# Performance work log

Measured on AMD Instinct MI355X. Metric: run time of the kernel, lower is better.

The kernel has to match this reference:

```python
import jax, jax.numpy as jnp
import numpy as np

EMB = 768
HEADS = 12
HEAD_DIM = EMB // HEADS
SEQ = 4096
BATCH = 1


def setup_inputs() -> dict:
    key = jax.random.key(0)
    ks = jax.random.split(key, 9)
    s = 1.0 / np.sqrt(EMB)
    return {
        "x": jax.random.normal(ks[0], (BATCH, SEQ, EMB), dtype=jnp.float32),
        "wq": jax.random.normal(ks[1], (EMB, EMB), dtype=jnp.float32) * s,
        "bq": jax.random.normal(ks[2], (EMB,), dtype=jnp.float32) * s,
        "wk": jax.random.normal(ks[3], (EMB, EMB), dtype=jnp.float32) * s,
        "bk": jax.random.normal(ks[4], (EMB,), dtype=jnp.float32) * s,
        "wv": jax.random.normal(ks[5], (EMB, EMB), dtype=jnp.float32) * s,
        "bv": jax.random.normal(ks[6], (EMB,), dtype=jnp.float32) * s,
        "wo": jax.random.normal(ks[7], (EMB, EMB), dtype=jnp.float32) * s,
        "bo": jax.random.normal(ks[8], (EMB,), dtype=jnp.float32) * s,
    }


def reference(x, wq, bq, wk, bk, wv, bv, wo, bo):
    b, n, _ = x.shape
    # projections: [b, n, emb] -> [b, heads, n, head_dim]
    def split_heads(t):
        return t.reshape(b, n, HEADS, HEAD_DIM).transpose(0, 2, 1, 3)
    q = split_heads(x @ wq + bq)
    k = split_heads(x @ wk + bk)
    v = split_heads(x @ wv + bv)
    # full N x N scores (naive attention, as in the original)
    scores = jnp.einsum("bhqd,bhkd->bhqk", q, k)
    causal = jnp.triu(jnp.ones((n, n), dtype=bool), k=1)
    scores = jnp.where(causal, -jnp.inf, scores)
    weights = jax.nn.softmax(scores / np.sqrt(HEAD_DIM), axis=-1)
    # dropout with rate 0.0 is identity (eval mode)
    ctx = jnp.einsum("bhqk,bhkd->bhqd", weights, v)
    ctx = ctx.transpose(0, 2, 1, 3).reshape(b, n, EMB)
    return ctx @ wo + bo
```

## Files before the change

### kernel.cpp

```cpp
#include <hip/hip_runtime.h>
#include <stdint.h>

#define SEQ 4096
#define EMB 768
#define HEADS 12
#define HD 64

typedef __attribute__((ext_vector_type(8))) short short8;
typedef __attribute__((ext_vector_type(4))) short short4v;
typedef __attribute__((ext_vector_type(8))) __bf16 bf16x8;
typedef __attribute__((ext_vector_type(4))) __bf16 bf16x4;
typedef __attribute__((ext_vector_type(4))) float f32x4;

#define QSCALE 0.18033688011112043f

static __device__ __forceinline__ unsigned short f2bf(float f) {
    unsigned int u = __builtin_bit_cast(unsigned int, f);
    unsigned int r = 0x7fffu + ((u >> 16) & 1u);
    u += r;
    return (unsigned short)(u >> 16);
}

static __device__ __forceinline__ f32x4 mfma32(short8 a, short8 b, f32x4 c) {
    return __builtin_amdgcn_mfma_f32_16x16x32_bf16(
        __builtin_bit_cast(bf16x8, a), __builtin_bit_cast(bf16x8, b), c, 0, 0, 0);
}

static __device__ __forceinline__ f32x4 mfma16(short4v a, short4v b, f32x4 c) {
#if __has_builtin(__builtin_amdgcn_mfma_f32_16x16x16_bf16)
    return __builtin_amdgcn_mfma_f32_16x16x16_bf16(
        __builtin_bit_cast(bf16x4, a), __builtin_bit_cast(bf16x4, b), c, 0, 0, 0);
#else
    return __builtin_amdgcn_mfma_f32_16x16x16bf16_1k(a, b, c, 0, 0, 0);
#endif
}

static __device__ __forceinline__ short4v pack4bf(float a, float b, float c, float d) {
#if __has_builtin(__builtin_amdgcn_cvt_pk_bf16_f32)
    typedef __attribute__((ext_vector_type(2))) __bf16 bf16x2;
    bf16x2 lo = __builtin_amdgcn_cvt_pk_bf16_f32(a, b);
    bf16x2 hi = __builtin_amdgcn_cvt_pk_bf16_f32(c, d);
    uint2 u = {__builtin_bit_cast(unsigned int, lo), __builtin_bit_cast(unsigned int, hi)};
    return __builtin_bit_cast(short4v, u);
#else
    short4v p;
    p[0] = (short)f2bf(a); p[1] = (short)f2bf(b);
    p[2] = (short)f2bf(c); p[3] = (short)f2bf(d);
    return p;
#endif
}

static __device__ __forceinline__ void load_lds16(const void* g, void* l) {
    __builtin_amdgcn_global_load_lds(
        (const __attribute__((address_space(1))) unsigned int*)(uintptr_t)g,
        (__attribute__((address_space(3))) unsigned int*)(uintptr_t)l, 16, 0, 0);
}

static __device__ __forceinline__ int pid_of(int h, int i128, int ch) {
    int b = (i128 < 20) ? (i128 - 10)
                        : (i128 < 30 ? 10 + (i128 - 20) * 2 : 30 + (i128 - 30) * 3);
    return h * 36 + b + (ch - 1);
}

static __device__ __forceinline__ void softmax_q(f32x4* st, float& m_i, float& l_i,
                                                 f32x4* O, short4v* pk) {
    float t0 = fmaxf(fmaxf(st[0][0], st[0][1]), fmaxf(st[0][2], st[0][3]));
    float t1 = fmaxf(fmaxf(st[1][0], st[1][1]), fmaxf(st[1][2], st[1][3]));
    float t2 = fmaxf(fmaxf(st[2][0], st[2][1]), fmaxf(st[2][2], st[2][3]));
    float t3 = fmaxf(fmaxf(st[3][0], st[3][1]), fmaxf(st[3][2], st[3][3]));
    float mx = fmaxf(fmaxf(t0, t1), fmaxf(t2, t3));
    if (__ballot(mx > m_i + 5.0f)) {
        mx = fmaxf(mx, __shfl_xor(mx, 16));
        mx = fmaxf(mx, __shfl_xor(mx, 32));
        const bool inc = mx > m_i;
        const float mn = inc ? mx : m_i;
        const float alpha = __builtin_amdgcn_exp2f(m_i - mn);
        m_i = mn;
        l_i *= alpha;
        for (int dt = 0; dt < 4; dt++)
            for (int r = 0; r < 4; r++) O[dt][r] *= alpha;
    }
    float rs = 0.f;
    for (int nt = 0; nt < 4; nt++) {
        float p0 = __builtin_amdgcn_exp2f(st[nt][0] - m_i);
        float p1 = __builtin_amdgcn_exp2f(st[nt][1] - m_i);
        float p2 = __builtin_amdgcn_exp2f(st[nt][2] - m_i);
        float p3 = __builtin_amdgcn_exp2f(st[nt][3] - m_i);
        rs += p0 + p1 + p2 + p3;
        pk[nt] = pack4bf(p0, p1, p2, p3);
    }
    l_i += rs;
}

__global__ __launch_bounds__(256) void convert_all(const float* __restrict__ x,
                                                   const float* __restrict__ wq,
                                                   const float* __restrict__ wk,
                                                   const float* __restrict__ wv,
                                                   const float* __restrict__ wo,
                                                   unsigned short* __restrict__ xb,
                                                   unsigned short* __restrict__ wqkvT,
                                                   unsigned short* __restrict__ woT) {
    __shared__ float Ls[64][65];
    const int bid = blockIdx.x;
    if (bid < 3072) {
        int i = bid * 256 + threadIdx.x;
        float4 v = ((const float4*)x)[i];
        ushort4 o = {f2bf(v.x), f2bf(v.y), f2bf(v.z), f2bf(v.w)};
        ((ushort4*)xb)[i] = o;
        return;
    }
    const int idx = bid - 3072;
    const int z = idx / 144;
    const int bx = (idx % 144) / 12, by = idx % 12;
    const float* W = (z == 0) ? wq : (z == 1) ? wk : (z == 2) ? wv : wo;
    unsigned short* dst = (z < 3) ? (wqkvT + (size_t)z * EMB * EMB) : woT;
    const int k0 = bx * 64, n0 = by * 64;
    const int r = threadIdx.x >> 2, c0 = (threadIdx.x & 3) * 16;
    for (int j = 0; j < 16; j += 4) {
        float4 v = *(const float4*)&W[(size_t)(k0 + r) * EMB + n0 + c0 + j];
        Ls[r][c0 + j] = v.x;
        Ls[r][c0 + j + 1] = v.y;
        Ls[r][c0 + j + 2] = v.z;
        Ls[r][c0 + j + 3] = v.w;
    }
    __syncthreads();
    unsigned short tmp[16];
    for (int j = 0; j < 16; j++) tmp[j] = f2bf(Ls[c0 + j][r]);
    *(uint4*)&dst[(size_t)(n0 + r) * EMB + k0 + c0] = *(uint4*)tmp;
    *(uint4*)&dst[(size_t)(n0 + r) * EMB + k0 + c0 + 8] = *(uint4*)(tmp + 8);
}

__global__ __launch_bounds__(256) void gemm_qkv(const unsigned short* __restrict__ A,
                                                const unsigned short* __restrict__ Bt,
                                                const float* __restrict__ b0p,
                                                const float* __restrict__ b1p,
                                                const float* __restrict__ b2p,
                                                unsigned short* __restrict__ QKb,
                                                unsigned short* __restrict__ Vtb) {
    __shared__ __align__(16) unsigned short SMEM[16384];
    const int tid = threadIdx.x;
    const int wave = tid >> 6, lane = tid & 63, quad = lane >> 4, l16 = lane & 15;
    const int m0 = blockIdx.x * 128, n0 = blockIdx.y * 128;
    const int wm = (wave >> 1) * 64, wn = (wave & 1) * 64;
    const int lrow = lane >> 2, lcol = (lane & 3) * 8;

    f32x4 acc[4][4] = {};

    for (int t = 0; t < 2; t++) {
        int row = wave * 32 + t * 16 + lrow;
        load_lds16(&A[(size_t)(m0 + row) * EMB + lcol], &SMEM[(wave * 2 + t) * 512]);
        load_lds16(&Bt[(size_t)(n0 + row) * EMB + lcol], &SMEM[4096 + (wave * 2 + t) * 512]);
    }
    int buf = 0;
    for (int k0 = 0; k0 < EMB; k0 += 32) {
        __syncthreads();
        if (k0 + 32 < EMB) {
            unsigned short* A_ = &SMEM[(buf ^ 1) * 8192];
            unsigned short* B_ = A_ + 4096;
            for (int t = 0; t < 2; t++) {
                int row = wave * 32 + t * 16 + lrow;
                load_lds16(&A[(size_t)(m0 + row) * EMB + k0 + 32 + lcol], &A_[(wave * 2 + t) * 512]);
                load_lds16(&Bt[(size_t)(n0 + row) * EMB + k0 + 32 + lcol], &B_[(wave * 2 + t) * 512]);
            }
        }
        const unsigned short* A_ = &SMEM[buf * 8192];
        const unsigned short* B_ = A_ + 4096;
        short8 a[4], b[4];
        for (int i = 0; i < 4; i++) a[i] = *(const short8*)&A_[(wm + i * 16 + l16) * 32 + quad * 8];
        for (int i = 0; i < 4; i++) b[i] = *(const short8*)&B_[(wn + i * 16 + l16) * 32 + quad * 8];
        for (int i = 0; i < 4; i++)
            for (int j = 0; j < 4; j++) acc[i][j] = mfma32(a[i], b[j], acc[i][j]);
        buf ^= 1;
    }

    const int z = n0 / EMB;
    if (z < 2) {
        const float* bias = z ? b1p : b0p;
        const float sc = z ? 1.0f : QSCALE;
        for (int i = 0; i < 4; i++)
            for (int j = 0; j < 4; j++) {
                int mbase = m0 + wm + i * 16 + quad * 4;
                int n = n0 + wn + j * 16 + l16;
                float bv = bias[n - z * EMB];
                for (int r = 0; r < 4; r++)
                    QKb[(size_t)(mbase + r) * 1536 + n] = f2bf((acc[i][j][r] + bv) * sc);
            }
    } else {
        const int nn = n0 + wn + l16 - 2 * EMB;
        for (int j = 0; j < 4; j++) {
            __syncthreads();
            const float bv = b2p[nn + j * 16];
            const int nloc = (wave & 1) * 16 + l16;
            for (int i = 0; i < 4; i++) {
                ushort4 pk;
                pk.x = f2bf(acc[i][j][0] + bv);
                pk.y = f2bf(acc[i][j][1] + bv);
                pk.z = f2bf(acc[i][j][2] + bv);
                pk.w = f2bf(acc[i][j][3] + bv);
                *(ushort4*)&SMEM[nloc * 136 + wm + i * 16 + quad * 4] = pk;
            }
            __syncthreads();
            const int nl = tid >> 3, c = tid & 7;
            const int ng = (nl >> 4) * 64 + j * 16 + (nl & 15) + n0 - 2 * EMB;
            const int hh = ng >> 6, dd = ng & 63;
            unsigned short* dst = &Vtb[(size_t)(hh * HD + dd) * SEQ + m0];
            *(uint4*)&dst[c * 8] = *(uint4*)&SMEM[nl * 136 + c * 8];
            *(uint4*)&dst[64 + c * 8] = *(uint4*)&SMEM[nl * 136 + 64 + c * 8];
        }
    }
}

__global__ __launch_bounds__(256) void gemm_out(const unsigned short* __restrict__ A,
                                                const unsigned short* __restrict__ Bt,
                                                const float* __restrict__ bias,
                                                float* __restrict__ outp) {
    __shared__ __align__(16) unsigned short SMEM[12288];
    const int tid = threadIdx.x;
    const int wave = tid >> 6, lane = tid & 63, quad = lane >> 4, l16 = lane & 15;
    const int m0 = blockIdx.x * 64, n0 = blockIdx.y * 128;
    const int wm = (wave >> 1) * 32, wn = (wave & 1) * 64;
    const int lrow = lane >> 2, lcol = (lane & 3) * 8;

    f32x4 acc[2][4] = {};

    load_lds16(&A[(size_t)(m0 + wave * 16 + lrow) * EMB + lcol], &SMEM[wave * 512]);
    for (int t = 0; t < 2; t++) {
        int row = wave * 32 + t * 16 + lrow;
        load_lds16(&Bt[(size_t)(n0 + row) * EMB + lcol], &SMEM[4096 + (wave * 2 + t) * 512]);
    }
    int buf = 0;
    for (int k0 = 0; k0 < EMB; k0 += 32) {
        __syncthreads();
        if (k0 + 32 < EMB) {
            unsigned short* A_ = &SMEM[(buf ^ 1) * 2048];
            unsigned short* B_ = &SMEM[4096 + (buf ^ 1) * 4096];
            load_lds16(&A[(size_t)(m0 + wave * 16 + lrow) * EMB + k0 + 32 + lcol], &A_[wave * 512]);
            for (int t = 0; t < 2; t++) {
                int row = wave * 32 + t * 16 + lrow;
                load_lds16(&Bt[(size_t)(n0 + row) * EMB + k0 + 32 + lcol], &B_[(wave * 2 + t) * 512]);
            }
        }
        const unsigned short* A_ = &SMEM[buf * 2048];
        const unsigned short* B_ = &SMEM[4096 + buf * 4096];
        short8 a[2], b[4];
        for (int i = 0; i < 2; i++) a[i] = *(const short8*)&A_[(wm + i * 16 + l16) * 32 + quad * 8];
        for (int j = 0; j < 4; j++) b[j] = *(const short8*)&B_[(wn + j * 16 + l16) * 32 + quad * 8];
        for (int i = 0; i < 2; i++)
            for (int j = 0; j < 4; j++) acc[i][j] = mfma32(a[i], b[j], acc[i][j]);
        buf ^= 1;
    }

    for (int i = 0; i < 2; i++)
        for (int j = 0; j < 4; j++) {
            int mbase = m0 + wm + i * 16 + quad * 4;
            int n = n0 + wn + j * 16 + l16;
            float bv = bias[n];
            for (int r = 0; r < 4; r++) outp[(size_t)(mbase + r) * EMB + n] = acc[i][j][r] + bv;
        }
}

__global__ __launch_bounds__(256, 3) void attn_kernel(const unsigned short* __restrict__ QKb,
                                                      const unsigned short* __restrict__ Vtb,
                                                      unsigned short* __restrict__ ctxb,
                                                      unsigned short* __restrict__ Op,
                                                      float* __restrict__ mArr,
                                                      float* __restrict__ lArr) {
    __shared__ __align__(16) unsigned short Ks[64 * 64];
    __shared__ __align__(16) unsigned short Vs[2][64 * 64];

    const int bid = blockIdx.x;
    const int h = bid % HEADS;
    const int r2 = 67 - bid / HEADS;
    int i128, ch, nch;
    if (r2 < 10) {
        i128 = r2; ch = 0; nch = 1;
    } else if (r2 < 30) {
        int t = r2 - 10; i128 = 10 + (t >> 1); ch = t & 1; nch = 2;
    } else if (r2 < 60) {
        int t = r2 - 30; i128 = 20 + t / 3; ch = t % 3; nch = 3;
    } else {
        int t = r2 - 60; i128 = 30 + (t >> 2); ch = t & 3; nch = 4;
    }
    const int T = 2 * i128 + 2;
    const int kb = ch * T / nch;
    const int ke = (ch + 1) * T / nch - 1;
    const int qbase = i128 * 128;
    const int tid = threadIdx.x;
    const int wave = tid >> 6, lane = tid & 63, quad = lane >> 4, l16 = lane & 15;

    const unsigned short* Qg = QKb + (size_t)h * HD;
    const unsigned short* Kg = QKb + (size_t)(EMB + h * HD);
    const unsigned short* Vh = Vtb + (size_t)h * HD * SEQ;

    const int qa = qbase + wave * 32 + l16;
    const int qb = qa + 16;
    const short8 bQ0a = *(const short8*)&Qg[(size_t)qa * 1536 + quad * 8];
    const short8 bQ1a = *(const short8*)&Qg[(size_t)qa * 1536 + 32 + quad * 8];
    const short8 bQ0b = *(const short8*)&Qg[(size_t)qb * 1536 + quad * 8];
    const short8 bQ1b = *(const short8*)&Qg[(size_t)qb * 1536 + 32 + quad * 8];

    const int row = tid >> 2, t4 = tid & 3;
    const int swk = row & 7, swv = row & 15;

    f32x4 Oa[4] = {}, Ob[4] = {};
    float m_a = -3.0e38f, l_a = 0.f;
    float m_b = -3.0e38f, l_b = 0.f;

    uint4 kr0, kr1, vr0, vr1;
    {
        const int kb64 = kb * 64;
        const unsigned short* kp = &Kg[(size_t)(kb64 + row) * 1536];
        kr0 = *(const uint4*)&kp[(2 * t4) * 8];
        kr1 = *(const uint4*)&kp[(2 * t4 + 1) * 8];
        const unsigned short* vp = &Vh[(size_t)row * SEQ + kb64];
        vr0 = *(const uint4*)&vp[t4 * 16];
        vr1 = *(const uint4*)&vp[t4 * 16 + 8];
    }
    *(uint4*)&Ks[row * 64 + ((2 * t4) ^ swk) * 8] = kr0;
    *(uint4*)&Ks[row * 64 + ((2 * t4 + 1) ^ swk) * 8] = kr1;
    *(uint2*)&Vs[0][row * 64 + ((4 * t4) ^ swv) * 4] = ((const uint2*)&vr0)[0];
    *(uint2*)&Vs[0][row * 64 + ((4 * t4 + 1) ^ swv) * 4] = ((const uint2*)&vr0)[1];
    *(uint2*)&Vs[0][row * 64 + ((4 * t4 + 2) ^ swv) * 4] = ((const uint2*)&vr1)[0];
    *(uint2*)&Vs[0][row * 64 + ((4 * t4 + 3) ^ swv) * 4] = ((const uint2*)&vr1)[1];
    if (kb < ke) {
        const int nb = (kb + 1) * 64;
        const unsigned short* kp = &Kg[(size_t)(nb + row) * 1536];
        kr0 = *(const uint4*)&kp[(2 * t4) * 8];
        kr1 = *(const uint4*)&kp[(2 * t4 + 1) * 8];
        const unsigned short* vp = &Vh[(size_t)row * SEQ + nb];
        vr0 = *(const uint4*)&vp[t4 * 16];
        vr1 = *(const uint4*)&vp[t4 * 16 + 8];
    }
    __syncthreads();

    const int qw = qbase + wave * 32 + 31;
    const int swr = l16 & 7;

    f32x4 sa[4], sb[4];
    if (kb * 64 <= qw) {
        for (int nt = 0; nt < 4; nt++) {
            short8 aK0 = *(const short8*)&Ks[(nt * 16 + l16) * 64 + (quad ^ swr) * 8];
            short8 aK1 = *(const short8*)&Ks[(nt * 16 + l16) * 64 + ((quad + 4) ^ swr) * 8];
            f32x4 za = {};
            za = mfma32(aK0, bQ0a, za);
            za = mfma32(aK1, bQ1a, za);
            sa[nt] = za;
            f32x4 zb = {};
            zb = mfma32(aK0, bQ0b, zb);
            zb = mfma32(aK1, bQ1b, zb);
            sb[nt] = zb;
        }
        if (kb * 64 + 63 > qbase + wave * 32) {
            for (int nt = 0; nt < 4; nt++)
                for (int r = 0; r < 4; r++) {
                    const int kk = kb * 64 + nt * 16 + quad * 4 + r;
                    if (kk > qa) sa[nt][r] = -INFINITY;
                    if (kk > qb) sb[nt][r] = -INFINITY;
                }
        }
    }

    int p = 0;
    for (int kt = kb; kt <= ke; kt++) {
        __syncthreads();
        if (kt < ke) {
            *(uint4*)&Ks[row * 64 + ((2 * t4) ^ swk) * 8] = kr0;
            *(uint4*)&Ks[row * 64 + ((2 * t4 + 1) ^ swk) * 8] = kr1;
            *(uint2*)&Vs[p ^ 1][row * 64 + ((4 * t4) ^ swv) * 4] = ((const uint2*)&vr0)[0];
            *(uint2*)&Vs[p ^ 1][row * 64 + ((4 * t4 + 1) ^ swv) * 4] = ((const uint2*)&vr0)[1];
            *(uint2*)&Vs[p ^ 1][row * 64 + ((4 * t4 + 2) ^ swv) * 4] = ((const uint2*)&vr1)[0];
            *(uint2*)&Vs[p ^ 1][row * 64 + ((4 * t4 + 3) ^ swv) * 4] = ((const uint2*)&vr1)[1];
            if (kt + 1 < ke) {
                const int nb = (kt + 2) * 64;
                const unsigned short* kp = &Kg[(size_t)(nb + row) * 1536];
                kr0 = *(const uint4*)&kp[(2 * t4) * 8];
                kr1 = *(const uint4*)&kp[(2 * t4 + 1) * 8];
                const unsigned short* vp = &Vh[(size_t)row * SEQ + nb];
                vr0 = *(const uint4*)&vp[t4 * 16];
                vr1 = *(const uint4*)&vp[t4 * 16 + 8];
            }
        }
        __syncthreads();

        const int kbase = kt * 64;
        const bool cur = (kbase <= qw);

        short4v pka[4], pkb[4];
        if (cur) {
            softmax_q(sa, m_a, l_a, Oa, pka);
            softmax_q(sb, m_b, l_b, Ob, pkb);
        }

        const int kn = kbase + 64;
        if (kt < ke && kn <= qw) {
            for (int nt = 0; nt < 4; nt++) {
                short8 aK0 = *(const short8*)&Ks[(nt * 16 + l16) * 64 + (quad ^ swr) * 8];
                short8 aK1 = *(const short8*)&Ks[(nt * 16 + l16) * 64 + ((quad + 4) ^ swr) * 8];
                f32x4 za = {};
                za = mfma32(aK0, bQ0a, za);
                za = mfma32(aK1, bQ1a, za);
                sa[nt] = za;
                f32x4 zb = {};
                zb = mfma32(aK0, bQ0b, zb);
                zb = mfma32(aK1, bQ1b, zb);
                sb[nt] = zb;
            }
            if (kn + 63 > qbase + wave * 32) {
                for (int nt = 0; nt < 4; nt++)
                    for (int r = 0; r < 4; r++) {
                        const int kk = kn + nt * 16 + quad * 4 + r;
                        if (kk > qa) sa[nt][r] = -INFINITY;
                        if (kk > qb) sb[nt][r] = -INFINITY;
                    }
            }
        }

        if (cur) {
            for (int dt = 0; dt < 4; dt++)
                for (int nt = 0; nt < 4; nt++) {
                    short4v av =
                        *(const short4v*)&Vs[p][(dt * 16 + l16) * 64 + ((4 * nt + quad) ^ l16) * 4];
                    Oa[dt] = mfma16(av, pka[nt], Oa[dt]);
                    Ob[dt] = mfma16(av, pkb[nt], Ob[dt]);
                }
        }

        p ^= 1;
    }

    l_a += __shfl_xor(l_a, 16);
    l_a += __shfl_xor(l_a, 32);
    l_b += __shfl_xor(l_b, 16);
    l_b += __shfl_xor(l_b, 32);

    const int qla = wave * 32 + l16;
    const int qlb = qla + 16;
    if (nch == 1) {
        const float ia = 1.f / l_a, ib = 1.f / l_b;
        for (int dt = 0; dt < 4; dt++) {
            ushort4 oa, ob;
            oa.x = f2bf(Oa[dt][0] * ia);
            oa.y = f2bf(Oa[dt][1] * ia);
            oa.z = f2bf(Oa[dt][2] * ia);
            oa.w = f2bf(Oa[dt][3] * ia);
            ob.x = f2bf(Ob[dt][0] * ib);
            ob.y = f2bf(Ob[dt][1] * ib);
            ob.z = f2bf(Ob[dt][2] * ib);
            ob.w = f2bf(Ob[dt][3] * ib);
            *(ushort4*)&ctxb[(size_t)qa * EMB + h * HD + dt * 16 + quad * 4] = oa;
            *(ushort4*)&ctxb[(size_t)qb * EMB + h * HD + dt * 16 + quad * 4] = ob;
        }
    } else {
        if (ch == 0) {
            for (int dt = 0; dt < 4; dt++) {
                ushort4 oa, ob;
                oa.x = f2bf(Oa[dt][0]);
                oa.y = f2bf(Oa[dt][1]);
                oa.z = f2bf(Oa[dt][2]);
                oa.w = f2bf(Oa[dt][3]);
                ob.x = f2bf(Ob[dt][0]);
                ob.y = f2bf(Ob[dt][1]);
                ob.z = f2bf(Ob[dt][2]);
                ob.w = f2bf(Ob[dt][3]);
                *(ushort4*)&ctxb[(size_t)qa * EMB + h * HD + dt * 16 + quad * 4] = oa;
                *(ushort4*)&ctxb[(size_t)qb * EMB + h * HD + dt * 16 + quad * 4] = ob;
            }
        } else {
            const int pid = pid_of(h, i128, ch);
            for (int dt = 0; dt < 4; dt++) {
                ushort4 oa, ob;
                oa.x = f2bf(Oa[dt][0]);
                oa.y = f2bf(Oa[dt][1]);
                oa.z = f2bf(Oa[dt][2]);
                oa.w = f2bf(Oa[dt][3]);
                ob.x = f2bf(Ob[dt][0]);
                ob.y = f2bf(Ob[dt][1]);
                ob.z = f2bf(Ob[dt][2]);
                ob.w = f2bf(Ob[dt][3]);
                *(ushort4*)&Op[(size_t)pid * 8192 + qla * 64 + dt * 16 + quad * 4] = oa;
                *(ushort4*)&Op[(size_t)pid * 8192 + qlb * 64 + dt * 16 + quad * 4] = ob;
            }
        }
        if (quad == 0) {
            const int mlb = ((h * 32 + i128) * 4 + ch) * 128;
            mArr[mlb + qla] = m_a;
            lArr[mlb + qla] = l_a;
            mArr[mlb + qlb] = m_b;
            lArr[mlb + qlb] = l_b;
        }
    }
}

__global__ __launch_bounds__(256) void merge_kernel(const unsigned short* __restrict__ Op,
                                                    const float* __restrict__ mArr,
                                                    const float* __restrict__ lArr,
                                                    unsigned short* __restrict__ ctxb) {
    const int gid = blockIdx.x;
    const int h = gid % HEADS;
    const int i128 = 10 + gid / HEADS;
    const int nch = (i128 < 20) ? 2 : (i128 < 30) ? 3 : 4;
    const int q = threadIdx.x >> 1, d0 = (threadIdx.x & 1) * 32;
    const int mlbase = (h * 32 + i128) * 4;

    float mc[4], lc[4];
    for (int c = 0; c < nch; c++) {
        mc[c] = mArr[(mlbase + c) * 128 + q];
        lc[c] = lArr[(mlbase + c) * 128 + q];
    }
    float M = mc[0];
    for (int c = 1; c < nch; c++) M = fmaxf(M, mc[c]);
    float w[4], L = 0.f;
    for (int c = 0; c < nch; c++) {
        w[c] = __builtin_amdgcn_exp2f(mc[c] - M);
        L += w[c] * lc[c];
    }
    const float inv = 1.f / L;
    for (int c = 0; c < nch; c++) w[c] *= inv;

    unsigned short* dst = &ctxb[(size_t)(i128 * 128 + q) * EMB + h * HD + d0];
    for (int jj = 0; jj < 32; jj += 8) {
        uint4 u0 = *(const uint4*)&dst[jj];
        float f[8];
        const unsigned short* p0 = (const unsigned short*)&u0;
        for (int t = 0; t < 8; t++)
            f[t] = w[0] * __builtin_bit_cast(float, (unsigned int)p0[t] << 16);
        for (int c = 1; c < nch; c++) {
            const int pid = pid_of(h, i128, c);
            uint4 u = *(const uint4*)&Op[(size_t)pid * 8192 + q * 64 + d0 + jj];
            const unsigned short* p = (const unsigned short*)&u;
            for (int t = 0; t < 8; t++)
                f[t] += w[c] * __builtin_bit_cast(float, (unsigned int)p[t] << 16);
        }
        unsigned short o[8];
        for (int t = 0; t < 8; t++) o[t] = f2bf(f[t]);
        *(uint4*)&dst[jj] = *(uint4*)o;
    }
}

extern "C" void kernel_launch(void* const* d_in, const int* in_sizes, int n_in,
                              void* d_out, int out_size, void* d_ws, size_t ws_size,
                              hipStream_t stream) {
    const float* x = (const float*)d_in[0];
    const float* wq = (const float*)d_in[1];
    const float* bq = (const float*)d_in[2];
    const float* wk = (const float*)d_in[3];
    const float* bk = (const float*)d_in[4];
    const float* wv = (const float*)d_in[5];
    const float* bv = (const float*)d_in[6];
    const float* wo = (const float*)d_in[7];
    const float* bo = (const float*)d_in[8];

    unsigned short* ws = (unsigned short*)d_ws;
    unsigned short* xb = ws;
    unsigned short* wqkvT = xb + SEQ * EMB;
    unsigned short* woT = wqkvT + 3 * EMB * EMB;
    unsigned short* QKb = woT + EMB * EMB;
    unsigned short* Vtb = QKb + (size_t)SEQ * 1536;
    unsigned short* ctxb = Vtb + HEADS * SEQ * HD;
    unsigned short* Op = xb;
    float* mArr = (float*)(ws + 3538944);
    float* lArr = mArr + 196608;

    convert_all<<<dim3(3072 + 576), 256, 0, stream>>>(x, wq, wk, wv, wo, xb, wqkvT, woT);
    gemm_qkv<<<dim3(SEQ / 128, 3 * EMB / 128), 256, 0, stream>>>(
        xb, wqkvT, bq, bk, bv, QKb, Vtb);
    attn_kernel<<<dim3(12 * 68), 256, 0, stream>>>(QKb, Vtb, ctxb, Op, mArr, lArr);
    merge_kernel<<<dim3(264), 256, 0, stream>>>(Op, mArr, lArr, ctxb);
    gemm_out<<<dim3(SEQ / 64, EMB / 128), 256, 0, stream>>>(ctxb, woT, bo, (float*)d_out);
}
```

Baseline: 183.0 us.

## Split causal attention KV range into finer chunks when workspace allows

Adds a templated fine-grained split-KV mode that doubles the number of KV chunks per 128-row query block (2/4/6/8 instead of 1/2/3/4), launching 1632 attention blocks instead of 816. Partial outputs and m/l statistics go to a separate workspace region, and the merge kernel now covers all 32 query blocks per head. The aim is better load balance and occupancy across the GPU's compute units, at the cost of more partial-output traffic and extra merge work. The fine path is selected only when the workspace is large enough.

```diff
diff --git a/kernel.cpp b/kernel.cpp
--- a/kernel.cpp
+++ b/kernel.cpp
@@ -56,10 +56,18 @@
         (__attribute__((address_space(3))) unsigned int*)(uintptr_t)l, 16, 0, 0);
 }
 
-static __device__ __forceinline__ int pid_of(int h, int i128, int ch) {
+static __device__ __forceinline__ int pid_coarse(int h, int i128, int ch) {
     int b = (i128 < 20) ? (i128 - 10)
                         : (i128 < 30 ? 10 + (i128 - 20) * 2 : 30 + (i128 - 30) * 3);
     return h * 36 + b + (ch - 1);
+}
+
+static __device__ __forceinline__ int pid_fine(int h, int i128, int ch) {
+    int b = (i128 < 10) ? i128
+          : (i128 < 20) ? 10 + (i128 - 10) * 3
+          : (i128 < 30) ? 40 + (i128 - 20) * 5
+                        : 90 + (i128 - 30) * 7;
+    return h * 104 + b + (ch - 1);
 }
 
 static __device__ __forceinline__ void softmax_q(f32x4* st, float& m_i, float& l_i,
@@ -259,6 +267,7 @@
         }
 }
 
+template <bool FINE>
 __global__ __launch_bounds__(256, 3) void attn_kernel(const unsigned short* __restrict__ QKb,
                                                       const unsigned short* __restrict__ Vtb,
                                                       unsigned short* __restrict__ ctxb,
@@ -270,16 +279,29 @@
 
     const int bid = blockIdx.x;
     const int h = bid % HEADS;
-    const int r2 = 67 - bid / HEADS;
     int i128, ch, nch;
-    if (r2 < 10) {
-        i128 = r2; ch = 0; nch = 1;
-    } else if (r2 < 30) {
-        int t = r2 - 10; i128 = 10 + (t >> 1); ch = t & 1; nch = 2;
-    } else if (r2 < 60) {
-        int t = r2 - 30; i128 = 20 + t / 3; ch = t % 3; nch = 3;
+    if (FINE) {
+        const int r2 = 135 - bid / HEADS;
+        if (r2 < 20) {
+            i128 = r2 >> 1; ch = r2 & 1; nch = 2;
+        } else if (r2 < 60) {
+            int t = r2 - 20; i128 = 10 + (t >> 2); ch = t & 3; nch = 4;
+        } else if (r2 < 120) {
+            int t = r2 - 60; i128 = 20 + t / 6; ch = t % 6; nch = 6;
+        } else {
+            int t = r2 - 120; i128 = 30 + (t >> 3); ch = t & 7; nch = 8;
+        }
     } else {
-        int t = r2 - 60; i128 = 30 + (t >> 2); ch = t & 3; nch = 4;
+        const int r2 = 67 - bid / HEADS;
+        if (r2 < 10) {
+            i128 = r2; ch = 0; nch = 1;
+        } else if (r2 < 30) {
+            int t = r2 - 10; i128 = 10 + (t >> 1); ch = t & 1; nch = 2;
+        } else if (r2 < 60) {
+            int t = r2 - 30; i128 = 20 + t / 3; ch = t % 3; nch = 3;
+        } else {
+            int t = r2 - 60; i128 = 30 + (t >> 2); ch = t & 3; nch = 4;
+        }
     }
     const int T = 2 * i128 + 2;
     const int kb = ch * T / nch;
@@ -435,7 +457,7 @@
 
     const int qla = wave * 32 + l16;
     const int qlb = qla + 16;
-    if (nch == 1) {
+    if (!FINE && nch == 1) {
         const float ia = 1.f / l_a, ib = 1.f / l_b;
         for (int dt = 0; dt < 4; dt++) {
             ushort4 oa, ob;
@@ -466,7 +488,7 @@
                 *(ushort4*)&ctxb[(size_t)qb * EMB + h * HD + dt * 16 + quad * 4] = ob;
             }
         } else {
-            const int pid = pid_of(h, i128, ch);
+            const int pid = FINE ? pid_fine(h, i128, ch) : pid_coarse(h, i128, ch);
             for (int dt = 0; dt < 4; dt++) {
                 ushort4 oa, ob;
                 oa.x = f2bf(Oa[dt][0]);
@@ -482,7 +504,8 @@
             }
         }
         if (quad == 0) {
-            const int mlb = ((h * 32 + i128) * 4 + ch) * 128;
+            const int MLS = FINE ? 8 : 4;
+            const int mlb = ((h * 32 + i128) * MLS + ch) * 128;
             mArr[mlb + qla] = m_a;
             lArr[mlb + qla] = l_a;
             mArr[mlb + qlb] = m_b;
@@ -491,25 +514,31 @@
     }
 }
 
+template <bool FINE>
 __global__ __launch_bounds__(256) void merge_kernel(const unsigned short* __restrict__ Op,
                                                     const float* __restrict__ mArr,
                                                     const float* __restrict__ lArr,
                                                     unsigned short* __restrict__ ctxb) {
     const int gid = blockIdx.x;
     const int h = gid % HEADS;
-    const int i128 = 10 + gid / HEADS;
-    const int nch = (i128 < 20) ? 2 : (i128 < 30) ? 3 : 4;
+    const int i128 = FINE ? (gid / HEADS) : (10 + gid / HEADS);
+    int nch;
+    if (FINE)
+        nch = (i128 < 10) ? 2 : (i128 < 20) ? 4 : (i128 < 30) ? 6 : 8;
+    else
+        nch = (i128 < 20) ? 2 : (i128 < 30) ? 3 : 4;
+    const int MLS = FINE ? 8 : 4;
     const int q = threadIdx.x >> 1, d0 = (threadIdx.x & 1) * 32;
-    const int mlbase = (h * 32 + i128) * 4;
-
-    float mc[4], lc[4];
+    const int mlbase = (h * 32 + i128) * MLS;
+
+    float mc[8], lc[8];
     for (int c = 0; c < nch; c++) {
         mc[c] = mArr[(mlbase + c) * 128 + q];
         lc[c] = lArr[(mlbase + c) * 128 + q];
     }
     float M = mc[0];
     for (int c = 1; c < nch; c++) M = fmaxf(M, mc[c]);
-    float w[4], L = 0.f;
+    float w[8], L = 0.f;
     for (int c = 0; c < nch; c++) {
         w[c] = __builtin_amdgcn_exp2f(mc[c] - M);
         L += w[c] * lc[c];
@@ -525,7 +554,7 @@
         for (int t = 0; t < 8; t++)
             f[t] = w[0] * __builtin_bit_cast(float, (unsigned int)p0[t] << 16);
         for (int c = 1; c < nch; c++) {
-            const int pid = pid_of(h, i128, c);
+            const int pid = FINE ? pid_fine(h, i128, c) : pid_coarse(h, i128, c);
             uint4 u = *(const uint4*)&Op[(size_t)pid * 8192 + q * 64 + d0 + jj];
             const unsigned short* p = (const unsigned short*)&u;
             for (int t = 0; t < 8; t++)
@@ -557,14 +586,24 @@
     unsigned short* QKb = woT + EMB * EMB;
     unsigned short* Vtb = QKb + (size_t)SEQ * 1536;
     unsigned short* ctxb = Vtb + HEADS * SEQ * HD;
-    unsigned short* Op = xb;
-    float* mArr = (float*)(ws + 3538944);
-    float* lArr = mArr + 196608;
 
     convert_all<<<dim3(3072 + 576), 256, 0, stream>>>(x, wq, wk, wv, wo, xb, wqkvT, woT);
     gemm_qkv<<<dim3(SEQ / 128, 3 * EMB / 128), 256, 0, stream>>>(
         xb, wqkvT, bq, bk, bv, QKb, Vtb);
-    attn_kernel<<<dim3(12 * 68), 256, 0, stream>>>(QKb, Vtb, ctxb, Op, mArr, lArr);
-    merge_kernel<<<dim3(264), 256, 0, stream>>>(Op, mArr, lArr, ctxb);
+
+    const bool fine = ws_size >= (size_t)29884416 * 2;
+    if (fine) {
+        unsigned short* OpF = ws + 18087936u;
+        float* mF = (float*)(ws + 28311552u);
+        float* lF = mF + 393216;
+        attn_kernel<true><<<dim3(12 * 136), 256, 0, stream>>>(QKb, Vtb, ctxb, OpF, mF, lF);
+        merge_kernel<true><<<dim3(12 * 32), 256, 0, stream>>>(OpF, mF, lF, ctxb);
+    } else {
+        unsigned short* Op = xb;
+        float* mArr = (float*)(ws + 3538944);
+        float* lArr = mArr + 196608;
+        attn_kernel<false><<<dim3(12 * 68), 256, 0, stream>>>(QKb, Vtb, ctxb, Op, mArr, lArr);
+        merge_kernel<false><<<dim3(264), 256, 0, stream>>>(Op, mArr, lArr, ctxb);
+    }
     gemm_out<<<dim3(SEQ / 64, EMB / 128), 256, 0, stream>>>(ctxb, woT, bo, (float*)d_out);
 }
```

After: 191.1 us. +4.4%, slower.
